# Performance work log

Hardware: AMD Instinct MI355X
Metric: run time of the kernel (lower is better)

The kernel has to match this reference:

```python
import jax, jax.numpy as jnp
import numpy as np

B, N, M = 32, 8400, 32
NUM_CLASSES = 80
TOP_K = 10
CLS_W, OBJ_W, REG_W = 1.0, 1.0, 5.0
EPS = 1e-7
IMG = 640.0


def setup_inputs() -> dict:
    key = jax.random.key(0)
    k1, k2, k3, k4, k5, k6, k7 = jax.random.split(key, 7)
    # decoded predictions in pixel scale: [cx, cy, w, h, obj_logit, cls_logits...]
    cxy = jax.random.uniform(k1, (B, N, 2), jnp.float32, 0.0, IMG)
    wh = jax.random.uniform(k2, (B, N, 2), jnp.float32, 10.0, 110.0)
    obj = jax.random.normal(k3, (B, N, 1), jnp.float32)
    cls = jax.random.normal(k4, (B, N, NUM_CLASSES), jnp.float32)
    predictions = jnp.concatenate([cxy, wh, obj, cls], axis=-1)  # (B, N, 85)
    # targets: [cls, cx, cy, w, h]
    gcls = jnp.floor(jax.random.uniform(k5, (B, M, 1), jnp.float32, 0.0, float(NUM_CLASSES)))
    gxy = jax.random.uniform(k6, (B, M, 2), jnp.float32, 50.0, IMG - 50.0)
    gwh = jax.random.uniform(k7, (B, M, 2), jnp.float32, 20.0, 120.0)
    targets = jnp.concatenate([gcls, gxy, gwh], axis=-1)  # (B, M, 5)
    return {"predictions": predictions, "targets": targets}


def cxcywh_to_xyxy(b):
    cx, cy, w, h = b[..., 0], b[..., 1], b[..., 2], b[..., 3]
    return jnp.stack([cx - w / 2, cy - h / 2, cx + w / 2, cy + h / 2], axis=-1)


def bce_with_logits(x, t):
    # numerically stable elementwise BCE with logits
    return jnp.maximum(x, 0.0) - x * t + jnp.log1p(jnp.exp(-jnp.abs(x)))


def pairwise_iou(g, p):
    # g: (M,4) xyxy, p: (N,4) xyxy -> (M,N)
    ix1 = jnp.maximum(g[:, None, 0], p[None, :, 0])
    iy1 = jnp.maximum(g[:, None, 1], p[None, :, 1])
    ix2 = jnp.minimum(g[:, None, 2], p[None, :, 2])
    iy2 = jnp.minimum(g[:, None, 3], p[None, :, 3])
    inter = jnp.clip(ix2 - ix1, 0.0) * jnp.clip(iy2 - iy1, 0.0)
    ga = jnp.clip(g[:, 2] - g[:, 0], 0.0) * jnp.clip(g[:, 3] - g[:, 1], 0.0)
    pa = jnp.clip(p[:, 2] - p[:, 0], 0.0) * jnp.clip(p[:, 3] - p[:, 1], 0.0)
    union = ga[:, None] + pa[None, :] - inter + EPS
    return inter / union


def giou(pred, tgt):
    # elementwise GIoU, pred/tgt (N,4) xyxy -> (N,)
    ix1 = jnp.maximum(pred[:, 0], tgt[:, 0]); iy1 = jnp.maximum(pred[:, 1], tgt[:, 1])
    ix2 = jnp.minimum(pred[:, 2], tgt[:, 2]); iy2 = jnp.minimum(pred[:, 3], tgt[:, 3])
    inter = jnp.clip(ix2 - ix1, 0.0) * jnp.clip(iy2 - iy1, 0.0)
    pa = jnp.clip(pred[:, 2] - pred[:, 0], 0.0) * jnp.clip(pred[:, 3] - pred[:, 1], 0.0)
    ta = jnp.clip(tgt[:, 2] - tgt[:, 0], 0.0) * jnp.clip(tgt[:, 3] - tgt[:, 1], 0.0)
    union = pa + ta - inter + EPS
    iou = inter / union
    ex1 = jnp.minimum(pred[:, 0], tgt[:, 0]); ey1 = jnp.minimum(pred[:, 1], tgt[:, 1])
    ex2 = jnp.maximum(pred[:, 2], tgt[:, 2]); ey2 = jnp.maximum(pred[:, 3], tgt[:, 3])
    enclose = (ex2 - ex1) * (ey2 - ey1) + EPS
    return iou - (enclose - union) / enclose


def _image_loss(pred, tgt):
    # pred: (N, 5+C), tgt: (M, 5)
    pbox = pred[:, :4]
    obj_logit = pred[:, 4]
    cls_logit = pred[:, 5:]
    pxyxy = cxcywh_to_xyxy(pbox)
    gcls = tgt[:, 0].astype(jnp.int32)                  # (M,)
    gxyxy = cxcywh_to_xyxy(tgt[:, 1:5])                 # (M,4)

    iou = pairwise_iou(gxyxy, pxyxy)                    # (M,N)

    # center prior: anchor (prediction) centers inside GT boxes
    cx, cy = pbox[:, 0], pbox[:, 1]
    in_box = ((cx[None, :] > gxyxy[:, 0:1]) & (cx[None, :] < gxyxy[:, 2:3]) &
              (cy[None, :] > gxyxy[:, 1:2]) & (cy[None, :] < gxyxy[:, 3:4]))  # (M,N)

    # classification cost: BCE(sqrt(cls_p*obj_p), onehot), decomposed to avoid (M,N,C)
    score = jnp.sqrt(jax.nn.sigmoid(cls_logit) * jax.nn.sigmoid(obj_logit)[:, None])  # (N,C)
    lp = jnp.log(score + EPS)
    lq = jnp.log(1.0 - score + EPS)
    base = -lq.sum(axis=-1)                             # (N,) = sum_c BCE(p, 0)
    cost_cls = base[None, :] - lp[:, gcls].T + lq[:, gcls].T  # (M,N)

    reg_cost = -jnp.log(iou + 1e-8)
    cost = cost_cls + 3.0 * reg_cost + 1e5 * (~in_box).astype(pred.dtype)
    cost = jax.lax.stop_gradient(cost)

    # dynamic-k: k_m = clip(sum of top-k IoUs, min 1)
    iou_sg = jax.lax.stop_gradient(iou) * in_box.astype(pred.dtype)
    topk_ious, _ = jax.lax.top_k(iou_sg, TOP_K)         # (M, TOP_K)
    dyn_k = jnp.clip(topk_ious.sum(-1).astype(jnp.int32), 1, None)  # (M,)

    # per-GT: keep the dyn_k lowest-cost candidates (rank via double argsort)
    ranks = jnp.argsort(jnp.argsort(cost, axis=1), axis=1)
    assigned = (ranks < dyn_k[:, None]) & in_box        # (M,N)

    # conflict resolution: anchor keeps only its lowest-cost GT
    big = jnp.asarray(1e30, pred.dtype)
    cost_masked = jnp.where(assigned, cost, big)
    matched_gt = jnp.argmin(cost_masked, axis=0)        # (N,)
    fg = assigned.any(axis=0)                            # (N,)
    fgf = fg.astype(pred.dtype)

    # objectness loss over all anchors
    obj_l = bce_with_logits(obj_logit, fgf).sum()
    # classification loss on foreground anchors
    onehot = jax.nn.one_hot(gcls[matched_gt], NUM_CLASSES, dtype=pred.dtype)
    cls_l = (bce_with_logits(cls_logit, onehot) * fgf[:, None]).sum()
    mbox = gxyxy[matched_gt]                            # (N,4)
    reg_l = ((1.0 - giou(pxyxy, mbox)) * fgf).sum()
    return cls_l, obj_l, reg_l, fgf.sum()


def reference(predictions, targets):
    cls_l, obj_l, reg_l, nfg = jax.vmap(_image_loss)(predictions, targets)
    num_fg = jnp.maximum(nfg.sum(), 1.0)
    total = (CLS_W * cls_l.sum() + OBJ_W * obj_l.sum() + REG_W * reg_l.sum()) / num_fg
    return total
```

## Files before the change

kernel.cpp:

```cpp
#include <hip/hip_runtime.h>
#include <math.h>

#define BB 32
#define NN 8400
#define MM 32
#define NC 80
#define PD 85
#define TOPK 10
#define CAPG 768
#define KPL 12
#define NBLK 1050
#define FLT_BIG 3.4e38f

__device__ __forceinline__ float frcp_(float x)  { return __builtin_amdgcn_rcpf(x); }
__device__ __forceinline__ float fsqrt_(float x) { return __builtin_amdgcn_sqrtf(x); }
__device__ __forceinline__ float fsig_(float x)  { return frcp_(1.0f + __expf(-x)); }

__device__ __forceinline__ float bcef_(float x, float t) {
    return fmaxf(x, 0.0f) - x * t + __logf(1.0f + __expf(-fabsf(x)));
}

__device__ __forceinline__ float iou_(float4 pb, float gx1, float gy1,
                                      float gx2, float gy2, float ga) {
    float ix1 = fmaxf(gx1, pb.x), iy1 = fmaxf(gy1, pb.y);
    float ix2 = fminf(gx2, pb.z), iy2 = fminf(gy2, pb.w);
    float inter = fmaxf(ix2 - ix1, 0.0f) * fmaxf(iy2 - iy1, 0.0f);
    float pa = fmaxf(pb.z - pb.x, 0.0f) * fmaxf(pb.w - pb.y, 0.0f);
    float uni = ga + pa - inter + 1e-7f;
    return inter * frcp_(uni);
}
__device__ __forceinline__ float cost_(float cl, float so_n, float base_n, float iou) {
    float s = fsqrt_(fsig_(cl) * so_n);
    float lp = __logf(s + 1e-7f);
    float lq = __logf(1.0f - s + 1e-7f);
    return base_n - lp + lq - 3.0f * __logf(iou + 1e-8f);
}

__global__ void __launch_bounds__(256) kA(const float* __restrict__ pred,
                                          const float* __restrict__ tgt,
                                          float4* __restrict__ pxyxy,
                                          float* __restrict__ base,
                                          float* __restrict__ so,
                                          float* __restrict__ objlogit,
                                          unsigned int* __restrict__ inmask,
                                          unsigned int* __restrict__ mask) {
    const int tid = threadIdx.x;
    const int lane = tid & 63, wid = tid >> 6;
    const int b = blockIdx.y;
    const int r = blockIdx.x * 256 + tid;

    __shared__ float4 sg[MM];
    __shared__ int s_act[256];
    __shared__ int s_wb[4];
    __shared__ int s_na;

    if (tid < MM) {
        const float* t = tgt + ((size_t)b * MM + tid) * 5;
        sg[tid] = make_float4(t[1] - t[3] * 0.5f, t[2] - t[4] * 0.5f,
                              t[1] + t[3] * 0.5f, t[2] + t[4] * 0.5f);
    }
    __syncthreads();

    const bool valid = r < NN;
    unsigned int im = 0u;
    if (valid) {
        const size_t gi = (size_t)b * NN + r;
        const float* p = pred + gi * PD;
        float4 h4 = *reinterpret_cast<const float4*>(p);
        float ol = p[4];
        float cx = h4.x, cy = h4.y, w = h4.z, h = h4.w;
        #pragma unroll
        for (int g = 0; g < MM; ++g) {
            float4 gb = sg[g];
            bool inb = (cx > gb.x) && (cx < gb.z) && (cy > gb.y) && (cy < gb.w);
            im |= inb ? (1u << g) : 0u;
        }
        pxyxy[gi] = make_float4(cx - w * 0.5f, cy - h * 0.5f,
                                cx + w * 0.5f, cy + h * 0.5f);
        objlogit[gi] = ol;
        so[gi] = fsig_(ol);
        inmask[gi] = im;
        mask[gi] = 0u;
    }

    unsigned long long bal = __ballot(valid && im != 0u);
    int wpos = __popcll(bal & ((1ull << lane) - 1ull));
    if (lane == 0) s_wb[wid] = __popcll(bal);
    __syncthreads();
    if (tid == 0) {
        int acc = 0;
        for (int w2 = 0; w2 < 4; ++w2) { int t2 = s_wb[w2]; s_wb[w2] = acc; acc += t2; }
        s_na = acc;
    }
    __syncthreads();
    if (valid && im != 0u) s_act[s_wb[wid] + wpos] = r;
    __syncthreads();

    const int na = s_na;
    for (int idx = wid; idx < na; idx += 4) {
        const int ar = s_act[idx];
        const size_t off = ((size_t)b * NN + ar) * PD;
        float x0 = pred[off + lane];
        float x1 = (lane < 21) ? pred[off + 64 + lane] : 0.0f;
        float so_r = fsig_(__shfl(x0, 4));
        float a = 0.0f;
        if (lane >= 5) a += __logf(1.0f - fsqrt_(fsig_(x0) * so_r) + 1e-7f);
        if (lane < 21) a += __logf(1.0f - fsqrt_(fsig_(x1) * so_r) + 1e-7f);
        #pragma unroll
        for (int o = 32; o; o >>= 1) a += __shfl_xor(a, o);
        if (lane == 0) base[(size_t)b * NN + ar] = -a;
    }
}

__global__ void __launch_bounds__(256) kC(const float* __restrict__ pred,
                                          const float* __restrict__ tgt,
                                          const float4* __restrict__ pxyxy,
                                          const float* __restrict__ base,
                                          const float* __restrict__ so,
                                          const unsigned int* __restrict__ inmask,
                                          unsigned int* __restrict__ mask) {
    const int x_ = blockIdx.x & 7, k_ = blockIdx.x >> 3;
    const int g = k_ & 31, b = ((k_ >> 5) << 3) | x_;
    const int tid = threadIdx.x;
    const int wid = tid >> 6, lane = tid & 63;

    const float* t = tgt + ((size_t)b * MM + g) * 5;
    const int gcls = (int)t[0];
    const float gx1 = t[1] - t[3] * 0.5f, gy1 = t[2] - t[4] * 0.5f;
    const float gx2 = t[1] + t[3] * 0.5f, gy2 = t[2] + t[4] * 0.5f;
    const float ga = fmaxf(gx2 - gx1, 0.0f) * fmaxf(gy2 - gy1, 0.0f);
    const size_t nb = (size_t)b * NN;
    const unsigned int gbit = 1u << g;

    __shared__ float s_iou[CAPG];
    __shared__ float s_cost[CAPG];
    __shared__ int   s_n[CAPG];
    __shared__ int   s_cnt;
    if (tid == 0) s_cnt = 0;
    __syncthreads();

    #define KC_BODY(nn_)                                                       \
        do { int n = (nn_);                                                    \
            float4 pb = pxyxy[nb + n];                                         \
            float iou = iou_(pb, gx1, gy1, gx2, gy2, ga);                      \
            float cl = pred[(nb + (size_t)n) * PD + 5 + gcls];                 \
            float co = cost_(cl, so[nb + n], base[nb + n], iou);               \
            int idx = atomicAdd(&s_cnt, 1);                                    \
            if (idx < CAPG) { s_iou[idx] = iou; s_cost[idx] = co; s_n[idx] = n; } \
        } while (0)

    for (int n4 = tid; n4 < NN; n4 += 1024) {
        unsigned int m0 = inmask[nb + n4];
        unsigned int m1 = (n4 + 256 < NN) ? inmask[nb + n4 + 256] : 0u;
        unsigned int m2 = (n4 + 512 < NN) ? inmask[nb + n4 + 512] : 0u;
        unsigned int m3 = (n4 + 768 < NN) ? inmask[nb + n4 + 768] : 0u;
        if (m0 & gbit) KC_BODY(n4);
        if (m1 & gbit) KC_BODY(n4 + 256);
        if (m2 & gbit) KC_BODY(n4 + 512);
        if (m3 & gbit) KC_BODY(n4 + 768);
    }
    #undef KC_BODY
    __syncthreads();

    if (wid != 0) return;
    const int cnt = min(s_cnt, CAPG);

    float riou[KPL], rcost[KPL]; int rn[KPL];
    #pragma unroll
    for (int k = 0; k < KPL; ++k) {
        int i = lane + 64 * k;
        bool v = i < cnt;
        riou[k]  = v ? s_iou[i]  : -1.0f;
        rcost[k] = v ? s_cost[i] : FLT_BIG;
        rn[k]    = v ? s_n[i]    : 0x7fffffff;
    }

    float ssum = 0.0f;
    {
        const int lim = (cnt < TOPK) ? cnt : TOPK;
        for (int p = 0; p < lim; ++p) {
            float bv = -1.0f; int bidx = 0x7fffffff;
            #pragma unroll
            for (int k = 0; k < KPL; ++k)
                if (riou[k] > bv) { bv = riou[k]; bidx = lane + 64 * k; }
            #pragma unroll
            for (int o = 32; o; o >>= 1) {
                float ov = __shfl_xor(bv, o); int oi = __shfl_xor(bidx, o);
                if (ov > bv || (ov == bv && oi < bidx)) { bv = ov; bidx = oi; }
            }
            ssum += bv;
            if ((bidx & 63) == lane) {
                int kk = bidx >> 6;
                #pragma unroll
                for (int k = 0; k < KPL; ++k) if (k == kk) riou[k] = -1.0f;
            }
        }
    }
    int dynk = (int)ssum;
    if (dynk < 1) dynk = 1;
    if (dynk > TOPK) dynk = TOPK;

    {
        const int lim = (cnt < dynk) ? cnt : dynk;
        for (int p = 0; p < lim; ++p) {
            float bv = FLT_BIG; int bn_ = 0x7fffffff; int bidx = -1;
            #pragma unroll
            for (int k = 0; k < KPL; ++k)
                if (rcost[k] < bv || (rcost[k] == bv && rn[k] < bn_)) {
                    bv = rcost[k]; bn_ = rn[k]; bidx = lane + 64 * k;
                }
            #pragma unroll
            for (int o = 32; o; o >>= 1) {
                float ov = __shfl_xor(bv, o);
                int on = __shfl_xor(bn_, o);
                int oi = __shfl_xor(bidx, o);
                if (ov < bv || (ov == bv && on < bn_)) { bv = ov; bn_ = on; bidx = oi; }
            }
            if ((bidx & 63) == lane) {
                int kk = bidx >> 6;
                #pragma unroll
                for (int k = 0; k < KPL; ++k)
                    if (k == kk) { rcost[k] = FLT_BIG; rn[k] = 0x7fffffff; }
            }
            if (lane == 0) atomicOr(&mask[nb + bn_], gbit);
        }
    }
}

__global__ void __launch_bounds__(256) kD(const float* __restrict__ pred,
                   const float* __restrict__ tgt,
                   const float4* __restrict__ pxyxy,
                   const float* __restrict__ base,
                   const float* __restrict__ so,
                   const float* __restrict__ objlogit,
                   const unsigned int* __restrict__ mask,
                   float* __restrict__ partials) {
    const int tid = threadIdx.x;
    const int i0 = blockIdx.x * 256;
    const int i = i0 + tid;
    const int lane = tid & 63, wid = tid >> 6;
    const int b = i / NN;

    float obj_l, cls_l = 0.0f, reg_l = 0.0f, nfg = 0.0f;
    const unsigned int mk = mask[i];
    obj_l = bcef_(objlogit[i], mk ? 1.0f : 0.0f);

    __shared__ int s_list[256];
    __shared__ int s_gcls[256];
    __shared__ int s_wbase[4];
    __shared__ int s_cnt;

    unsigned long long bal = __ballot(mk != 0);
    int wpos = __popcll(bal & ((1ull << lane) - 1ull));
    if (lane == 0) s_wbase[wid] = __popcll(bal);
    __syncthreads();
    if (tid == 0) {
        int acc = 0;
        for (int w = 0; w < 4; ++w) { int t_ = s_wbase[w]; s_wbase[w] = acc; acc += t_; }
        s_cnt = acc;
    }
    __syncthreads();

    if (mk) {
        int e = s_wbase[wid] + wpos;
        s_list[e] = tid;
        nfg = 1.0f;
        float4 pb = pxyxy[i];
        float base_n = base[i], so_n = so[i];
        float best = 3.0e30f; int bg = 0;
        unsigned int m = mk;
        while (m) {
            int g = __ffs(m) - 1;
            m &= m - 1;
            const float* tg = tgt + ((size_t)b * MM + g) * 5;
            float ggx1 = tg[1] - tg[3] * 0.5f, ggy1 = tg[2] - tg[4] * 0.5f;
            float ggx2 = tg[1] + tg[3] * 0.5f, ggy2 = tg[2] + tg[4] * 0.5f;
            float gga = fmaxf(ggx2 - ggx1, 0.0f) * fmaxf(ggy2 - ggy1, 0.0f);
            float iou = iou_(pb, ggx1, ggy1, ggx2, ggy2, gga);
            float cl = pred[(size_t)i * PD + 5 + (int)tg[0]];
            float cvv = cost_(cl, so_n, base_n, iou);
            if (cvv < best) { best = cvv; bg = g; }
        }
        const float* tm = tgt + ((size_t)b * MM + bg) * 5;
        s_gcls[e] = (int)tm[0];
        float px1 = pb.x, py1 = pb.y, px2 = pb.z, py2 = pb.w;
        float tx1 = tm[1] - tm[3] * 0.5f, ty1 = tm[2] - tm[4] * 0.5f;
        float tx2 = tm[1] + tm[3] * 0.5f, ty2 = tm[2] + tm[4] * 0.5f;
        float ix1 = fmaxf(px1, tx1), iy1 = fmaxf(py1, ty1);
        float ix2 = fminf(px2, tx2), iy2 = fminf(py2, ty2);
        float inter = fmaxf(ix2 - ix1, 0.0f) * fmaxf(iy2 - iy1, 0.0f);
        float pa = fmaxf(px2 - px1, 0.0f) * fmaxf(py2 - py1, 0.0f);
        float ta = fmaxf(tx2 - tx1, 0.0f) * fmaxf(ty2 - ty1, 0.0f);
        float uni = pa + ta - inter + 1e-7f;
        float iou = inter / uni;
        float ex1 = fminf(px1, tx1), ey1 = fminf(py1, ty1);
        float ex2 = fmaxf(px2, tx2), ey2 = fmaxf(py2, ty2);
        float enclose = (ex2 - ex1) * (ey2 - ey1) + 1e-7f;
        float giou = iou - (enclose - uni) / enclose;
        reg_l = 1.0f - giou;
    }
    __syncthreads();

    const int cnt = s_cnt;
    const int nitems = cnt * NC;
    for (int item = tid; item < nitems; item += 256) {
        int e = item / NC;
        int c = item - e * NC;
        int gi = i0 + s_list[e];
        float x = pred[(size_t)gi * PD + 5 + c];
        cls_l += bcef_(x, (c == s_gcls[e]) ? 1.0f : 0.0f);
    }

    float sums[4] = {cls_l, obj_l, reg_l, nfg};
    #pragma unroll
    for (int j = 0; j < 4; ++j)
        #pragma unroll
        for (int o = 32; o; o >>= 1) sums[j] += __shfl_xor(sums[j], o);
    __shared__ float sred[16];
    if (lane == 0) {
        sred[wid * 4 + 0] = sums[0]; sred[wid * 4 + 1] = sums[1];
        sred[wid * 4 + 2] = sums[2]; sred[wid * 4 + 3] = sums[3];
    }
    __syncthreads();
    if (tid == 0) {
        float* pr = partials + (size_t)blockIdx.x * 4;
        #pragma unroll
        for (int j = 0; j < 4; ++j)
            pr[j] = sred[j] + sred[4 + j] + sred[8 + j] + sred[12 + j];
    }
}

__global__ void kE(const float* __restrict__ partials, int nblk, float* __restrict__ out) {
    __shared__ float red[256];
    float s[4] = {0, 0, 0, 0};
    for (int i = threadIdx.x; i < nblk; i += 256) {
        s[0] += partials[(size_t)i * 4 + 0];
        s[1] += partials[(size_t)i * 4 + 1];
        s[2] += partials[(size_t)i * 4 + 2];
        s[3] += partials[(size_t)i * 4 + 3];
    }
    float tot[4];
    for (int j = 0; j < 4; ++j) {
        red[threadIdx.x] = s[j];
        __syncthreads();
        for (int off = 128; off > 0; off >>= 1) {
            if (threadIdx.x < off) red[threadIdx.x] += red[threadIdx.x + off];
            __syncthreads();
        }
        tot[j] = red[0];
        __syncthreads();
    }
    if (threadIdx.x == 0) {
        float nfg = fmaxf(tot[3], 1.0f);
        out[0] = (tot[0] + tot[1] + 5.0f * tot[2]) / nfg;
    }
}

extern "C" void kernel_launch(void* const* d_in, const int* in_sizes, int n_in,
                              void* d_out, int out_size, void* d_ws, size_t ws_size,
                              hipStream_t stream) {
    const float* pred = (const float*)d_in[0];
    const float* tgt  = (const float*)d_in[1];
    float* out = (float*)d_out;

    char* ws = (char*)d_ws;
    size_t off = 0;
    float4* pxyxy = (float4*)(ws + off);            off += (size_t)BB * NN * sizeof(float4);
    float* base = (float*)(ws + off);               off += (size_t)BB * NN * sizeof(float);
    float* so = (float*)(ws + off);                 off += (size_t)BB * NN * sizeof(float);
    float* objlogit = (float*)(ws + off);           off += (size_t)BB * NN * sizeof(float);
    unsigned int* inmask = (unsigned int*)(ws + off); off += (size_t)BB * NN * sizeof(unsigned int);
    unsigned int* mask = (unsigned int*)(ws + off); off += (size_t)BB * NN * sizeof(unsigned int);
    float* partials = (float*)(ws + off);           off += (size_t)NBLK * 4 * sizeof(float);

    dim3 gA((NN + 255) / 256, BB);
    kA<<<gA, 256, 0, stream>>>(pred, tgt, pxyxy, base, so, objlogit, inmask, mask);

    kC<<<MM * BB, 256, 0, stream>>>(pred, tgt, pxyxy, base, so, inmask, mask);

    kD<<<NBLK, 256, 0, stream>>>(pred, tgt, pxyxy, base, so, objlogit, mask, partials);

    kE<<<1, 256, 0, stream>>>(partials, NBLK, out);
}
```

Measured before the change: 82.89 us.

## Process four GTs per kC block to share anchor scans and loads

kC now handles four ground-truth boxes per block of 512 threads instead of one GT per 256-thread block, so the grid shrinks from 1024 blocks to 256. The inmask scan and the per-anchor loads of box, so and base are shared across the four GTs, and each of the first four waves then runs the top-k and dynamic-k selection for one GT. This cuts redundant passes over the per-image mask, at the cost of fewer blocks in flight, about 36KB of shared memory per block, and a serial loop over GT bits per anchor.

```diff
diff --git a/kernel.cpp b/kernel.cpp
--- a/kernel.cpp
+++ b/kernel.cpp
@@ -112,67 +112,81 @@
     }
 }
 
-__global__ void __launch_bounds__(256) kC(const float* __restrict__ pred,
+__global__ void __launch_bounds__(512) kC(const float* __restrict__ pred,
                                           const float* __restrict__ tgt,
                                           const float4* __restrict__ pxyxy,
                                           const float* __restrict__ base,
                                           const float* __restrict__ so,
                                           const unsigned int* __restrict__ inmask,
                                           unsigned int* __restrict__ mask) {
-    const int x_ = blockIdx.x & 7, k_ = blockIdx.x >> 3;
-    const int g = k_ & 31, b = ((k_ >> 5) << 3) | x_;
+    const int b = blockIdx.x & 31, gq = blockIdx.x >> 5;
+    const int g0 = gq * 4;
     const int tid = threadIdx.x;
     const int wid = tid >> 6, lane = tid & 63;
-
-    const float* t = tgt + ((size_t)b * MM + g) * 5;
-    const int gcls = (int)t[0];
-    const float gx1 = t[1] - t[3] * 0.5f, gy1 = t[2] - t[4] * 0.5f;
-    const float gx2 = t[1] + t[3] * 0.5f, gy2 = t[2] + t[4] * 0.5f;
-    const float ga = fmaxf(gx2 - gx1, 0.0f) * fmaxf(gy2 - gy1, 0.0f);
     const size_t nb = (size_t)b * NN;
-    const unsigned int gbit = 1u << g;
-
-    __shared__ float s_iou[CAPG];
-    __shared__ float s_cost[CAPG];
-    __shared__ int   s_n[CAPG];
-    __shared__ int   s_cnt;
-    if (tid == 0) s_cnt = 0;
-    __syncthreads();
-
-    #define KC_BODY(nn_)                                                       \
-        do { int n = (nn_);                                                    \
-            float4 pb = pxyxy[nb + n];                                         \
-            float iou = iou_(pb, gx1, gy1, gx2, gy2, ga);                      \
-            float cl = pred[(nb + (size_t)n) * PD + 5 + gcls];                 \
-            float co = cost_(cl, so[nb + n], base[nb + n], iou);               \
-            int idx = atomicAdd(&s_cnt, 1);                                    \
-            if (idx < CAPG) { s_iou[idx] = iou; s_cost[idx] = co; s_n[idx] = n; } \
+
+    __shared__ float4 s_box[4];
+    __shared__ float s_ga[4];
+    __shared__ int s_gc[4];
+    __shared__ float s_iou[4][CAPG];
+    __shared__ float s_cost[4][CAPG];
+    __shared__ int   s_n[4][CAPG];
+    __shared__ int   s_cnt[4];
+    if (tid < 4) {
+        const float* t = tgt + ((size_t)b * MM + g0 + tid) * 5;
+        float x1 = t[1] - t[3] * 0.5f, y1 = t[2] - t[4] * 0.5f;
+        float x2 = t[1] + t[3] * 0.5f, y2 = t[2] + t[4] * 0.5f;
+        s_box[tid] = make_float4(x1, y1, x2, y2);
+        s_ga[tid] = fmaxf(x2 - x1, 0.0f) * fmaxf(y2 - y1, 0.0f);
+        s_gc[tid] = (int)t[0];
+        s_cnt[tid] = 0;
+    }
+    __syncthreads();
+
+    #define KC_BODY(nn_, mw_)                                                  \
+        do { unsigned int mm = ((mw_) >> g0) & 0xFu;                           \
+            if (mm) { int n = (nn_);                                           \
+                float4 pb = pxyxy[nb + n];                                     \
+                float so_n = so[nb + n], base_n = base[nb + n];                \
+                const float* prow = pred + (nb + (size_t)n) * PD + 5;          \
+                while (mm) {                                                   \
+                    int j = __ffs(mm) - 1; mm &= mm - 1;                       \
+                    float4 gb = s_box[j];                                      \
+                    float iou = iou_(pb, gb.x, gb.y, gb.z, gb.w, s_ga[j]);     \
+                    float co = cost_(prow[s_gc[j]], so_n, base_n, iou);        \
+                    int idx = atomicAdd(&s_cnt[j], 1);                         \
+                    if (idx < CAPG) { s_iou[j][idx] = iou; s_cost[j][idx] = co;\
+                                      s_n[j][idx] = n; }                       \
+                }                                                              \
+            }                                                                  \
         } while (0)
 
-    for (int n4 = tid; n4 < NN; n4 += 1024) {
+    for (int n4 = tid; n4 < NN; n4 += 2048) {
         unsigned int m0 = inmask[nb + n4];
-        unsigned int m1 = (n4 + 256 < NN) ? inmask[nb + n4 + 256] : 0u;
-        unsigned int m2 = (n4 + 512 < NN) ? inmask[nb + n4 + 512] : 0u;
-        unsigned int m3 = (n4 + 768 < NN) ? inmask[nb + n4 + 768] : 0u;
-        if (m0 & gbit) KC_BODY(n4);
-        if (m1 & gbit) KC_BODY(n4 + 256);
-        if (m2 & gbit) KC_BODY(n4 + 512);
-        if (m3 & gbit) KC_BODY(n4 + 768);
+        unsigned int m1 = (n4 + 512 < NN) ? inmask[nb + n4 + 512] : 0u;
+        unsigned int m2 = (n4 + 1024 < NN) ? inmask[nb + n4 + 1024] : 0u;
+        unsigned int m3 = (n4 + 1536 < NN) ? inmask[nb + n4 + 1536] : 0u;
+        KC_BODY(n4, m0);
+        KC_BODY(n4 + 512, m1);
+        KC_BODY(n4 + 1024, m2);
+        KC_BODY(n4 + 1536, m3);
     }
     #undef KC_BODY
     __syncthreads();
 
-    if (wid != 0) return;
-    const int cnt = min(s_cnt, CAPG);
+    if (wid >= 4) return;
+    const int j = wid;
+    const unsigned int gbit = 1u << (g0 + j);
+    const int cnt = min(s_cnt[j], CAPG);
 
     float riou[KPL], rcost[KPL]; int rn[KPL];
     #pragma unroll
     for (int k = 0; k < KPL; ++k) {
         int i = lane + 64 * k;
         bool v = i < cnt;
-        riou[k]  = v ? s_iou[i]  : -1.0f;
-        rcost[k] = v ? s_cost[i] : FLT_BIG;
-        rn[k]    = v ? s_n[i]    : 0x7fffffff;
+        riou[k]  = v ? s_iou[j][i]  : -1.0f;
+        rcost[k] = v ? s_cost[j][i] : FLT_BIG;
+        rn[k]    = v ? s_n[j][i]    : 0x7fffffff;
     }
 
     float ssum = 0.0f;
@@ -376,7 +390,7 @@
     dim3 gA((NN + 255) / 256, BB);
     kA<<<gA, 256, 0, stream>>>(pred, tgt, pxyxy, base, so, objlogit, inmask, mask);
 
-    kC<<<MM * BB, 256, 0, stream>>>(pred, tgt, pxyxy, base, so, inmask, mask);
+    kC<<<BB * 8, 512, 0, stream>>>(pred, tgt, pxyxy, base, so, inmask, mask);
 
     kD<<<NBLK, 256, 0, stream>>>(pred, tgt, pxyxy, base, so, objlogit, mask, partials);
 
```

After: 83.23 us. About the same (+0.4%).
